# Kernel optimization log

Measured on AMD Instinct MI355X. Metric: run time of the kernel, lower is better.

## Reference

```python
import jax, jax.numpy as jnp
import numpy as np

N_DST = 25000
E = 400000
DN = 128   # dim_node
DE = 128   # dim_edge
DT = 128   # dim_time
DO = 128   # dim_out
H = 2      # num_head


def setup_inputs() -> dict:
    key = jax.random.key(0)
    ks = jax.random.split(key, 10)
    sc = 0.05
    node_h = jax.random.normal(ks[0], (N_DST + E, DN), jnp.float32)
    edge_f = jax.random.normal(ks[1], (E, DE), jnp.float32)
    dt = jax.random.uniform(ks[2], (E,), jnp.float32) * 100.0
    dst_idx = jax.random.randint(ks[3], (E,), 0, N_DST)
    # TimeEncode: Linear(1, dim_time) with w initialized to 1/10**linspace(0,9)
    time_w = jnp.asarray(1.0 / 10 ** np.linspace(0, 9, DT, dtype=np.float32))
    time_b = jnp.zeros((DT,), jnp.float32)
    Wq = jax.random.normal(ks[4], (DO, DN + DT), jnp.float32) * sc
    bq = jnp.zeros((DO,), jnp.float32)
    Wk = jax.random.normal(ks[5], (DO, DN + DE + DT), jnp.float32) * sc
    bk = jnp.zeros((DO,), jnp.float32)
    Wv = jax.random.normal(ks[6], (DO, DN + DE + DT), jnp.float32) * sc
    bv = jnp.zeros((DO,), jnp.float32)
    Wout = jax.random.normal(ks[7], (DO, DN + DO), jnp.float32) * sc
    bout = jnp.zeros((DO,), jnp.float32)
    gamma = jnp.ones((DO,), jnp.float32)
    beta = jnp.zeros((DO,), jnp.float32)
    return dict(node_h=node_h, edge_f=edge_f, dt=dt, dst_idx=dst_idx,
                time_w=time_w, time_b=time_b, Wq=Wq, bq=bq, Wk=Wk, bk=bk,
                Wv=Wv, bv=bv, Wout=Wout, bout=bout, gamma=gamma, beta=beta)


def reference(node_h, edge_f, dt, dst_idx, time_w, time_b,
              Wq, bq, Wk, bk, Wv, bv, Wout, bout, gamma, beta):
    num_dst = node_h.shape[0] - edge_f.shape[0]
    num_edges = edge_f.shape[0]
    tgt = node_h[:num_dst]            # [N, DN] target node embeddings
    src = node_h[num_dst:]            # [E, DN] per-edge source embeddings

    # TimeEncode: cos(w * dt + b)
    time_feats = jnp.cos(dt[:, None] * time_w[None, :] + time_b)          # [E, DT]
    zero_time = jnp.broadcast_to(jnp.cos(time_b), (num_dst, time_b.shape[0]))

    Qn = jnp.concatenate([tgt, zero_time], axis=1) @ Wq.T + bq            # [N, DO]
    kv_in = jnp.concatenate([src, edge_f, time_feats], axis=1)            # [E, DN+DE+DT]
    K = kv_in @ Wk.T + bk                                                 # [E, DO]
    V = kv_in @ Wv.T + bv                                                 # [E, DO]
    Q = Qn[dst_idx]                                                       # gather per edge

    d_head = Q.shape[1] // H
    Qh = Q.reshape(num_edges, H, d_head)
    Kh = K.reshape(num_edges, H, d_head)
    Vh = V.reshape(num_edges, H, d_head)

    score = jnp.sum(Qh * Kh, axis=2)                                      # [E, H]
    score = jnp.where(score >= 0, score, 0.2 * score)                     # LeakyReLU(0.2)

    # edge_softmax: segmented softmax over incoming edges of each dst node
    m = jax.ops.segment_max(score, dst_idx, num_segments=num_dst)
    m = jnp.where(jnp.isfinite(m), m, 0.0)                                # empty segments
    e = jnp.exp(score - m[dst_idx])
    s = jax.ops.segment_sum(e, dst_idx, num_segments=num_dst)
    att = e / s[dst_idx]                                                  # [E, H]

    Vw = (Vh * att[:, :, None]).reshape(num_edges, -1)                    # [E, DO]
    h = jax.ops.segment_sum(Vw, dst_idx, num_segments=num_dst)            # scatter-sum

    rst = jnp.concatenate([h, tgt], axis=1) @ Wout.T + bout               # [N, DO]
    rst = jax.nn.relu(rst)
    mu = jnp.mean(rst, axis=-1, keepdims=True)
    var = jnp.var(rst, axis=-1, keepdims=True)
    return (rst - mu) / jnp.sqrt(var + 1e-5) * gamma + beta
```

## Files before the change

### kernel.cpp

```cpp
#include <hip/hip_runtime.h>

#define N_DST 25000
#define E_NUM 400000

typedef __bf16 bf16x8 __attribute__((ext_vector_type(8)));
typedef __bf16 bf16x4 __attribute__((ext_vector_type(4)));
typedef __bf16 bf16x2 __attribute__((ext_vector_type(2)));
typedef float  f32x4  __attribute__((ext_vector_type(4)));

__device__ __forceinline__ float fast_cos(float x) {
  float r = x * 0.15915494309189535f;
  r = r - floorf(r);
  return __builtin_amdgcn_cosf(r);
}

__device__ __forceinline__ void gload_lds16(const void* g, void* l) {
  __builtin_amdgcn_global_load_lds(
      (const __attribute__((address_space(1))) unsigned int*)g,
      (__attribute__((address_space(3))) unsigned int*)l, 16, 0, 0);
}

#define PIPE_WAIT(S)                         \
  do {                                       \
    __builtin_amdgcn_sched_barrier(0);       \
    asm volatile(S ::: "memory");            \
    __builtin_amdgcn_sched_barrier(0);       \
    __builtin_amdgcn_s_barrier();            \
    __builtin_amdgcn_sched_barrier(0);       \
  } while (0)

__device__ __forceinline__ void pack_frag(const float* __restrict__ W0,
    const float* __restrict__ W1, int stride, int NC, int idx, __bf16* __restrict__ out) {
  int lane = idx & 63, fid = idx >> 6;
  int nfw = NC >> 6;
  int perks = nfw << 2;
  int ks = fid / perks, rem = fid - ks * perks;
  int w = rem / nfw, nf = rem - w * nfw;
  int n = w * (NC >> 2) + nf * 16 + (lane & 15);
  int g = (ks << 2) + (lane >> 4);
  const float* src = (W1 && n >= 128) ? (W1 + (size_t)(n - 128) * stride)
                                      : (W0 + (size_t)n * stride);
  const float4* s4 = reinterpret_cast<const float4*>(src + g * 8);
  float4 lo = s4[0], hi = s4[1];
  bf16x8 b;
  b[0]=(__bf16)lo.x; b[1]=(__bf16)lo.y; b[2]=(__bf16)lo.z; b[3]=(__bf16)lo.w;
  b[4]=(__bf16)hi.x; b[5]=(__bf16)hi.y; b[6]=(__bf16)hi.z; b[7]=(__bf16)hi.w;
  reinterpret_cast<bf16x8*>(out)[idx] = b;
}

__global__ __launch_bounds__(256) void prep_kernel(
    const float* __restrict__ Wq, const float* __restrict__ bq, const float* __restrict__ tb,
    const float* __restrict__ Wk, const float* __restrict__ Wv, const float* __restrict__ Wout,
    const int* __restrict__ dsti,
    float* __restrict__ cq, __bf16* __restrict__ Bq_kv, __bf16* __restrict__ Bq_q,
    __bf16* __restrict__ Bq_out, int* __restrict__ counts) {
  int b = blockIdx.x, tid = threadIdx.x;
  if (b == 0) {
    if (tid < 128) {
      float s = bq[tid];
      for (int j = 0; j < 128; ++j) s += cosf(tb[j]) * Wq[tid * 256 + 128 + j];
      cq[tid] = s;
    }
    return;
  }
  b -= 1;
  if (b < 48) { pack_frag(Wk, Wv, 384, 256, b * 256 + tid, Bq_kv); return; }
  b -= 48;
  if (b < 8)  { pack_frag(Wq, nullptr, 256, 128, b * 256 + tid, Bq_q); return; }
  b -= 8;
  if (b < 16) { pack_frag(Wout, nullptr, 256, 128, b * 256 + tid, Bq_out); return; }
  b -= 16;
  int e = b * 256 + tid;
  if (e < E_NUM) atomicAdd(&counts[dsti[e]], 1);
}

__global__ __launch_bounds__(1024) void scan_kernel(const int* __restrict__ counts,
    int* __restrict__ offs, int* __restrict__ cursor) {
  __shared__ int wpart[16];
  int tid = threadIdx.x, lane = tid & 63, wid = tid >> 6;
  int carry = 0;
  for (int base = 0; base < N_DST; base += 1024) {
    int idx = base + tid;
    int x = (idx < N_DST) ? counts[idx] : 0;
    int incl = x;
#pragma unroll
    for (int o = 1; o < 64; o <<= 1) {
      int y = __shfl_up(incl, o);
      if (lane >= o) incl += y;
    }
    if (lane == 63) wpart[wid] = incl;
    __syncthreads();
    if (wid == 0) {
      int v = (lane < 16) ? wpart[lane] : 0;
      int s = v;
#pragma unroll
      for (int o = 1; o < 16; o <<= 1) {
        int y = __shfl_up(s, o);
        if (lane >= o) s += y;
      }
      if (lane < 16) wpart[lane] = s;
    }
    __syncthreads();
    int woff = (wid > 0) ? wpart[wid - 1] : 0;
    int tot = wpart[15];
    if (idx < N_DST) {
      int v = carry + woff + incl - x;
      offs[idx] = v;
      cursor[idx] = v;
    }
    carry += tot;
    __syncthreads();
  }
  if (tid == 0) offs[N_DST] = carry;
}

__global__ __launch_bounds__(256) void fill_kernel(const int* __restrict__ dsti,
    int* __restrict__ cursor, int* __restrict__ pos) {
  int e = blockIdx.x * 256 + threadIdx.x;
  if (e < E_NUM) {
    int d = dsti[e];
    int p = atomicAdd(&cursor[d], 1);
    pos[e] = p;
  }
}

__global__ __launch_bounds__(256, 3) void kv_kernel(
    const float* __restrict__ node_h, const float* __restrict__ edge_f,
    const float* __restrict__ dtp, const float* __restrict__ tw, const float* __restrict__ tb,
    const __bf16* __restrict__ Bq,
    const float* __restrict__ bk, const float* __restrict__ bv,
    const int* __restrict__ dsti, const int* __restrict__ pos,
    const float* __restrict__ Qn,
    __bf16* __restrict__ Vout, float* __restrict__ score)
{
  __shared__ __align__(16) float Abuf[3][4096];
  __shared__ int Dlds[64];
  __shared__ int Plds[64];
  __shared__ float dts[64];
  __shared__ float twl[128];
  __shared__ float tbl[128];

  const int tid = threadIdx.x;
  const int e0 = blockIdx.x * 64;
  const int lane = tid & 63;
  const int w = tid >> 6;
  const int lrow = lane & 15;
  const int lk = lane >> 4;
  const int aswz = (lrow & 7) << 4;

  if (tid < 64) {
    Dlds[tid] = dsti[e0 + tid];
    Plds[tid] = pos[e0 + tid];
    dts[tid] = dtp[e0 + tid];
  } else if (tid < 192) {
    int j = tid - 64;
    twl[j] = tw[j];
    tbl[j] = tb[j];
  }
  __syncthreads();

  auto stage_mem = [&](int t, int bufi) {
    const char* base;
    if (t < 2) base = (const char*)(node_h + ((size_t)(N_DST + e0)) * 128 + t * 64);
    else       base = (const char*)(edge_f + (size_t)e0 * 128 + (t - 2) * 64);
#pragma unroll
    for (int i = 0; i < 4; ++i) {
      int g = w * 4 + i;
      int r = g * 4 + (lane >> 4);
      int srcoff = r * 512 + ((((lane & 15) << 4)) ^ ((r & 7) << 4));
      gload_lds16(base + srcoff, &Abuf[bufi][g * 256]);
    }
  };
  auto stage_cos = [&](int t, float* buf) {
    int r = tid >> 2;
    int j0 = (tid & 3) << 4;
    float d = dts[r];
    int swz = (r & 7) << 4;
    char* rowb = (char*)(buf + r * 64);
#pragma unroll
    for (int q = 0; q < 4; ++q) {
      f32x4 vv;
#pragma unroll
      for (int jj = 0; jj < 4; ++jj) {
        int J = (t - 4) * 64 + j0 + q * 4 + jj;
        vv[jj] = fast_cos(d * twl[J] + tbl[J]);
      }
      *reinterpret_cast<f32x4*>(rowb + (((j0 << 2) + (q << 4)) ^ swz)) = vv;
    }
  };

  f32x4 acc[4][4];
#pragma unroll
  for (int mf = 0; mf < 4; ++mf)
#pragma unroll
    for (int nf = 0; nf < 4; ++nf)
      acc[mf][nf] = (f32x4){0.f, 0.f, 0.f, 0.f};

  const bf16x8* __restrict__ Bw = reinterpret_cast<const bf16x8*>(Bq) + (size_t)(w * 4) * 64 + lane;

  auto ktile = [&](const float* buf, int t) {
#pragma unroll
    for (int ks = 0; ks < 2; ++ks) {
      int K32 = t * 2 + ks;
      bf16x8 b[4];
#pragma unroll
      for (int nf = 0; nf < 4; ++nf)
        b[nf] = Bw[((size_t)K32 * 16 + nf) * 64];
      bf16x8 a[4];
#pragma unroll
      for (int mf = 0; mf < 4; ++mf) {
        const char* rowb = (const char*)(buf + (mf * 16 + lrow) * 64);
        int cb = ks * 128 + lk * 32;
        f32x4 f0 = *reinterpret_cast<const f32x4*>(rowb + (cb ^ aswz));
        f32x4 f1 = *reinterpret_cast<const f32x4*>(rowb + ((cb + 16) ^ aswz));
        bf16x8 av;
#pragma unroll
        for (int j = 0; j < 4; ++j) {
          av[j] = (__bf16)f0[j];
          av[4 + j] = (__bf16)f1[j];
        }
        a[mf] = av;
      }
#pragma unroll
      for (int nf = 0; nf < 4; ++nf)
#pragma unroll
        for (int mf = 0; mf < 4; ++mf)
          acc[mf][nf] = __builtin_amdgcn_mfma_f32_16x16x32_bf16(a[mf], b[nf], acc[mf][nf], 0, 0, 0);
    }
  };

  stage_mem(0, 0);
  stage_mem(1, 1);
  PIPE_WAIT("s_waitcnt vmcnt(4)");
  stage_mem(2, 2); ktile(Abuf[0], 0);
  PIPE_WAIT("s_waitcnt vmcnt(4)");
  stage_mem(3, 0); ktile(Abuf[1], 1);
  PIPE_WAIT("s_waitcnt vmcnt(4)");
  stage_cos(4, Abuf[1]); ktile(Abuf[2], 2);
  PIPE_WAIT("s_waitcnt vmcnt(0) lgkmcnt(0)");
  stage_cos(5, Abuf[2]); ktile(Abuf[0], 3);
  PIPE_WAIT("s_waitcnt lgkmcnt(0)");
  ktile(Abuf[1], 4);
  ktile(Abuf[2], 5);

  char* Vlds = (char*)Abuf[0];
  if (w >= 2) {
#pragma unroll
    for (int nf = 0; nf < 4; ++nf) {
      int vcol = (w - 2) * 64 + nf * 16 + lrow;
      float bb = bv[vcol];
#pragma unroll
      for (int mf = 0; mf < 4; ++mf) {
#pragma unroll
        for (int r = 0; r < 4; ++r) {
          int row = mf * 16 + lk * 4 + r;
          *reinterpret_cast<__bf16*>(Vlds + row * 256 + ((vcol * 2) ^ ((row & 7) << 4))) =
              (__bf16)(acc[mf][nf][r] + bb);
        }
      }
    }
  } else {
    float bkv[4];
#pragma unroll
    for (int nf = 0; nf < 4; ++nf) bkv[nf] = bk[w * 64 + nf * 16 + lrow];
#pragma unroll
    for (int mf = 0; mf < 4; ++mf) {
#pragma unroll
      for (int r = 0; r < 4; ++r) {
        int row = mf * 16 + lk * 4 + r;
        const float* qrow = Qn + ((size_t)Dlds[row] << 7) + w * 64;
        float s = 0.f;
#pragma unroll
        for (int nf = 0; nf < 4; ++nf)
          s += (acc[mf][nf][r] + bkv[nf]) * qrow[nf * 16 + lrow];
        s += __shfl_xor(s, 1);
        s += __shfl_xor(s, 2);
        s += __shfl_xor(s, 4);
        s += __shfl_xor(s, 8);
        if (lrow == 0) {
          s = (s >= 0.f) ? s : 0.2f * s;
          score[((size_t)Plds[row] << 1) + w] = s;
        }
      }
    }
  }
  __syncthreads();
#pragma unroll
  for (int i = 0; i < 4; ++i) {
    int c = tid + i * 256;
    int r = c >> 4, cb = (c & 15) << 4;
    bf16x8 vv = *reinterpret_cast<const bf16x8*>(Vlds + r * 256 + (cb ^ ((r & 7) << 4)));
    *reinterpret_cast<bf16x8*>(Vout + (((size_t)Plds[r]) << 7) + (c & 15) * 8) = vv;
  }
}

template<int MODE>
__global__ __launch_bounds__(256, 4) void gemm_kernel(
    const float* __restrict__ A0, const float* __restrict__ A1,
    const float* __restrict__ dtp, const float* __restrict__ tw,
    const __bf16* __restrict__ Bq, const float* __restrict__ bias0,
    float* __restrict__ outF)
{
  constexpr int NC = 128;
  constexpr int NFRAGW = 2;
  __shared__ __align__(16) char Abuf[2][64 * 256];

  const int tid = threadIdx.x;
  const int e0 = blockIdx.x * 64;
  const int nv = min(64, N_DST - e0);
  const int srow = tid >> 5;
  const int sc4 = (tid & 31) << 2;

  const int lane = tid & 63;
  const int w = tid >> 6;
  const int nbase = w * (NC / 4);
  const int lrow = lane & 15;
  const int lk = lane >> 4;
  const int aswz = (lrow & 7) << 4;
  const bf16x8* __restrict__ Bw =
      reinterpret_cast<const bf16x8*>(Bq) + (size_t)(w * NFRAGW) * 64 + lane;

  f32x4 acc[4][NFRAGW];
#pragma unroll
  for (int mf = 0; mf < 4; ++mf)
#pragma unroll
    for (int nf = 0; nf < NFRAGW; ++nf)
      acc[mf][nf] = (f32x4){0.f, 0.f, 0.f, 0.f};

  auto issueA = [&](int t, float4 (&v)[8]) {
    const float* base = (t == 0) ? A0 : A1;
#pragma unroll
    for (int i = 0; i < 8; ++i) {
      int r = srow + i * 8;
      v[i] = (r < nv) ? *reinterpret_cast<const float4*>(base + (size_t)(e0 + r) * 128 + sc4)
                      : make_float4(0.f, 0.f, 0.f, 0.f);
    }
  };
  auto writeA = [&](char* buf, float4 (&v)[8]) {
#pragma unroll
    for (int i = 0; i < 8; ++i) {
      int r = srow + i * 8;
      bf16x4 b;
      b[0]=(__bf16)v[i].x; b[1]=(__bf16)v[i].y; b[2]=(__bf16)v[i].z; b[3]=(__bf16)v[i].w;
      *reinterpret_cast<bf16x4*>(buf + r * 256 + ((sc4 * 2) ^ ((r & 7) << 4))) = b;
    }
  };
  auto ktile = [&](const char* buf, int t) {
#pragma unroll
    for (int ks = 0; ks < 4; ++ks) {
      bf16x8 b[NFRAGW];
#pragma unroll
      for (int nf = 0; nf < NFRAGW; ++nf)
        b[nf] = Bw[((size_t)(t * 4 + ks) * 4 * NFRAGW + nf) * 64];
      bf16x8 a[4];
#pragma unroll
      for (int mf = 0; mf < 4; ++mf)
        a[mf] = *reinterpret_cast<const bf16x8*>(
            buf + (mf * 16 + lrow) * 256 + (((ks * 32 + lk * 8) * 2) ^ aswz));
#pragma unroll
      for (int nf = 0; nf < NFRAGW; ++nf)
#pragma unroll
        for (int mf = 0; mf < 4; ++mf)
          acc[mf][nf] = __builtin_amdgcn_mfma_f32_16x16x32_bf16(a[mf], b[nf], acc[mf][nf], 0, 0, 0);
    }
  };

  float4 v[8];
  issueA(0, v);
  writeA(Abuf[0], v);
  __syncthreads();
  if constexpr (MODE == 2) {
    issueA(1, v);
    ktile(Abuf[0], 0);
    writeA(Abuf[1], v);
    __syncthreads();
    ktile(Abuf[1], 1);
  } else {
    ktile(Abuf[0], 0);
  }

  if constexpr (MODE == 0) {
#pragma unroll
    for (int nf = 0; nf < NFRAGW; ++nf) {
      int col = nbase + nf * 16 + lrow;
      float bb = bias0[col];
#pragma unroll
      for (int mf = 0; mf < 4; ++mf) {
#pragma unroll
        for (int r = 0; r < 4; ++r) {
          int row = mf * 16 + lk * 4 + r;
          if (row < nv)
            outF[(size_t)(e0 + row) * 128 + col] = acc[mf][nf][r] + bb;
        }
      }
    }
  } else {
    const float* gammaP = dtp;
    const float* betaP = tw;
    float vals[NFRAGW][4][4];
#pragma unroll
    for (int nf = 0; nf < NFRAGW; ++nf) {
      float bb = bias0[nbase + nf * 16 + lrow];
#pragma unroll
      for (int mf = 0; mf < 4; ++mf)
#pragma unroll
        for (int r = 0; r < 4; ++r)
          vals[nf][mf][r] = fmaxf(acc[mf][nf][r] + bb, 0.f);
    }
    __syncthreads();
    float* sums = reinterpret_cast<float*>(Abuf[0]);
    float* sqs  = reinterpret_cast<float*>(Abuf[0]) + 256;
    float* stats = reinterpret_cast<float*>(Abuf[0]) + 512;
#pragma unroll
    for (int mf = 0; mf < 4; ++mf) {
#pragma unroll
      for (int r = 0; r < 4; ++r) {
        float s1 = vals[0][mf][r] + vals[1][mf][r];
        float s2 = vals[0][mf][r] * vals[0][mf][r] + vals[1][mf][r] * vals[1][mf][r];
#pragma unroll
        for (int o = 1; o < 16; o <<= 1) {
          s1 += __shfl_xor(s1, o);
          s2 += __shfl_xor(s2, o);
        }
        if (lrow == 0) {
          int row = mf * 16 + lk * 4 + r;
          sums[w * 64 + row] = s1;
          sqs[w * 64 + row] = s2;
        }
      }
    }
    __syncthreads();
    if (tid < 64) {
      float s = sums[tid] + sums[64 + tid] + sums[128 + tid] + sums[192 + tid];
      float q = sqs[tid] + sqs[64 + tid] + sqs[128 + tid] + sqs[192 + tid];
      float mean = s * (1.f / 128.f);
      float var = q * (1.f / 128.f) - mean * mean;
      stats[tid * 2] = mean;
      stats[tid * 2 + 1] = rsqrtf(var + 1e-5f);
    }
    __syncthreads();
#pragma unroll
    for (int nf = 0; nf < NFRAGW; ++nf) {
      int col = nbase + nf * 16 + lrow;
      float g = gammaP[col], bC = betaP[col];
#pragma unroll
      for (int mf = 0; mf < 4; ++mf) {
#pragma unroll
        for (int r = 0; r < 4; ++r) {
          int row = mf * 16 + lk * 4 + r;
          if (row < nv) {
            float mean = stats[row * 2], rs = stats[row * 2 + 1];
            outF[(size_t)(e0 + row) * 128 + col] = (vals[nf][mf][r] - mean) * rs * g + bC;
          }
        }
      }
    }
  }
}

__global__ __launch_bounds__(256) void agg_kernel(const int* __restrict__ offs,
    const float* __restrict__ score, const __bf16* __restrict__ V, float* __restrict__ h) {
  int d = blockIdx.x * 4 + (threadIdx.x >> 6);
  if (d >= N_DST) return;
  int lane = threadIdx.x & 63;
  int beg = offs[d], end = offs[d + 1];
  int n = end - beg;
  float m0 = -3.0e38f, m1 = -3.0e38f;
  for (int i = lane; i < n; i += 64) {
    float2 sc = *reinterpret_cast<const float2*>(score + 2 * (size_t)(beg + i));
    m0 = fmaxf(m0, sc.x); m1 = fmaxf(m1, sc.y);
  }
#pragma unroll
  for (int o = 32; o; o >>= 1) {
    m0 = fmaxf(m0, __shfl_xor(m0, o));
    m1 = fmaxf(m1, __shfl_xor(m1, o));
  }
  float s0 = 0.f, s1 = 0.f;
  for (int i = lane; i < n; i += 64) {
    float2 sc = *reinterpret_cast<const float2*>(score + 2 * (size_t)(beg + i));
    s0 += __expf(sc.x - m0); s1 += __expf(sc.y - m1);
  }
#pragma unroll
  for (int o = 32; o; o >>= 1) {
    s0 += __shfl_xor(s0, o);
    s1 += __shfl_xor(s1, o);
  }
  float inv0 = (n > 0) ? 1.f / s0 : 0.f;
  float inv1 = (n > 0) ? 1.f / s1 : 0.f;
  int q = lane >> 4, j = lane & 15;
  int hsel = j >> 3;
  float acc[8];
#pragma unroll
  for (int k2 = 0; k2 < 8; ++k2) acc[k2] = 0.f;
  for (int i0 = 0; i0 < n; i0 += 4) {
    int i = i0 + q;
    if (i < n) {
      size_t p = beg + i;
      float2 sc = *reinterpret_cast<const float2*>(score + 2 * p);
      float wgt = hsel ? __expf(sc.y - m1) * inv1 : __expf(sc.x - m0) * inv0;
      bf16x8 v = *reinterpret_cast<const bf16x8*>(V + (p << 7) + j * 8);
#pragma unroll
      for (int k2 = 0; k2 < 8; ++k2) acc[k2] += wgt * (float)v[k2];
    }
  }
#pragma unroll
  for (int k2 = 0; k2 < 8; ++k2) {
    acc[k2] += __shfl_xor(acc[k2], 16);
    acc[k2] += __shfl_xor(acc[k2], 32);
  }
  if (q == 0) {
    float4 lo = make_float4(acc[0], acc[1], acc[2], acc[3]);
    float4 hi = make_float4(acc[4], acc[5], acc[6], acc[7]);
    float* dst = h + ((size_t)d << 7) + j * 8;
    *reinterpret_cast<float4*>(dst) = lo;
    *reinterpret_cast<float4*>(dst + 4) = hi;
  }
}

extern "C" void kernel_launch(void* const* d_in, const int* in_sizes, int n_in,
                              void* d_out, int out_size, void* d_ws, size_t ws_size,
                              hipStream_t stream) {
  (void)in_sizes; (void)n_in; (void)out_size; (void)ws_size;
  const float* node_h = (const float*)d_in[0];
  const float* edge_f = (const float*)d_in[1];
  const float* dtp    = (const float*)d_in[2];
  const int*   dsti   = (const int*)d_in[3];
  const float* tw     = (const float*)d_in[4];
  const float* tb     = (const float*)d_in[5];
  const float* Wq     = (const float*)d_in[6];
  const float* bq     = (const float*)d_in[7];
  const float* Wk     = (const float*)d_in[8];
  const float* bk     = (const float*)d_in[9];
  const float* Wv     = (const float*)d_in[10];
  const float* bv     = (const float*)d_in[11];
  const float* Wout   = (const float*)d_in[12];
  const float* bout   = (const float*)d_in[13];
  const float* gamma  = (const float*)d_in[14];
  const float* beta   = (const float*)d_in[15];
  float* outp = (float*)d_out;

  size_t off = 0;
  auto take = [&](size_t nbytes) -> void* {
    void* r = (char*)d_ws + off;
    off += (nbytes + 255) & ~(size_t)255;
    return r;
  };
  __bf16* Bq_kv  = (__bf16*)take((size_t)12288 * 16);
  __bf16* Bq_q   = (__bf16*)take((size_t)2048 * 16);
  __bf16* Bq_out = (__bf16*)take((size_t)4096 * 16);
  float*  cq     = (float*)take(128 * 4);
  float*  Qn     = (float*)take((size_t)N_DST * 128 * 4);
  __bf16* Vbuf   = (__bf16*)take((size_t)E_NUM * 128 * 2);
  float*  score  = (float*)take((size_t)E_NUM * 2 * 4);
  int*    counts = (int*)take((size_t)N_DST * 4);
  int*    offs   = (int*)take((size_t)(N_DST + 1) * 4);
  int*    cursor = (int*)take((size_t)N_DST * 4);
  int*    pos    = (int*)take((size_t)E_NUM * 4);
  float*  hbuf   = (float*)take((size_t)N_DST * 128 * 4);

  hipMemsetAsync(counts, 0, (size_t)N_DST * 4, stream);

  const int count_blocks = (E_NUM + 255) / 256;
  prep_kernel<<<1 + 48 + 8 + 16 + count_blocks, 256, 0, stream>>>(
      Wq, bq, tb, Wk, Wv, Wout, dsti, cq, Bq_kv, Bq_q, Bq_out, counts);

  gemm_kernel<0><<<(N_DST + 63) / 64, 256, 0, stream>>>(node_h, nullptr, nullptr, nullptr,
      Bq_q, cq, Qn);

  scan_kernel<<<1, 1024, 0, stream>>>(counts, offs, cursor);
  fill_kernel<<<count_blocks, 256, 0, stream>>>(dsti, cursor, pos);

  kv_kernel<<<E_NUM / 64, 256, 0, stream>>>(node_h, edge_f, dtp, tw, tb,
      Bq_kv, bk, bv, dsti, pos, Qn, Vbuf, score);

  agg_kernel<<<(N_DST + 3) / 4, 256, 0, stream>>>(offs, score, Vbuf, hbuf);

  gemm_kernel<2><<<(N_DST + 63) / 64, 256, 0, stream>>>(hbuf, node_h, gamma, beta,
      Bq_out, bout, outp);
}
```

Baseline: 360.2 us.

## Load KV GEMM A-operands directly from global; split scan into three-phase parallel kernels

The KV kernel drops its triple-buffered LDS pipeline (global_load_lds with waitcnt/barrier staging) and instead reads the source and edge feature fragments straight from global memory into registers. The time-encoding cosines are precomputed once into a small bf16 LDS tile. This cuts LDS from 48KB to 16KB, which is meant to raise occupancy, but the direct loads are strided per row and may coalesce worse, with less explicit latency hiding. Separately, the single-block serial scan becomes a three-kernel reduce/offset/scan spread over 25 blocks, at the cost of two extra launches.

After: 468.6 us. +30.1%, slower.

```diff
diff --git a/kernel.cpp b/kernel.cpp
--- a/kernel.cpp
+++ b/kernel.cpp
@@ -13,21 +13,6 @@
   r = r - floorf(r);
   return __builtin_amdgcn_cosf(r);
 }
-
-__device__ __forceinline__ void gload_lds16(const void* g, void* l) {
-  __builtin_amdgcn_global_load_lds(
-      (const __attribute__((address_space(1))) unsigned int*)g,
-      (__attribute__((address_space(3))) unsigned int*)l, 16, 0, 0);
-}
-
-#define PIPE_WAIT(S)                         \
-  do {                                       \
-    __builtin_amdgcn_sched_barrier(0);       \
-    asm volatile(S ::: "memory");            \
-    __builtin_amdgcn_sched_barrier(0);       \
-    __builtin_amdgcn_s_barrier();            \
-    __builtin_amdgcn_sched_barrier(0);       \
-  } while (0)
 
 __device__ __forceinline__ void pack_frag(const float* __restrict__ W0,
     const float* __restrict__ W1, int stride, int NC, int idx, __bf16* __restrict__ out) {
@@ -74,44 +59,64 @@
   if (e < E_NUM) atomicAdd(&counts[dsti[e]], 1);
 }
 
-__global__ __launch_bounds__(1024) void scan_kernel(const int* __restrict__ counts,
-    int* __restrict__ offs, int* __restrict__ cursor) {
+__global__ __launch_bounds__(1024) void scanA_kernel(const int* __restrict__ counts,
+    int* __restrict__ bsum) {
+  __shared__ int wsum[16];
+  int tid = threadIdx.x;
+  int idx = blockIdx.x * 1024 + tid;
+  int s = (idx < N_DST) ? counts[idx] : 0;
+#pragma unroll
+  for (int o = 32; o; o >>= 1) s += __shfl_xor(s, o);
+  if ((tid & 63) == 0) wsum[tid >> 6] = s;
+  __syncthreads();
+  if (tid == 0) {
+    int t = 0;
+#pragma unroll
+    for (int i = 0; i < 16; ++i) t += wsum[i];
+    bsum[blockIdx.x] = t;
+  }
+}
+
+__global__ void scanB_kernel(const int* __restrict__ bsum, int* __restrict__ boff) {
+  if (threadIdx.x == 0) {
+    int c = 0;
+    for (int i = 0; i < 25; ++i) { boff[i] = c; c += bsum[i]; }
+    boff[25] = c;
+  }
+}
+
+__global__ __launch_bounds__(1024) void scanC_kernel(const int* __restrict__ counts,
+    const int* __restrict__ boff, int* __restrict__ offs, int* __restrict__ cursor) {
   __shared__ int wpart[16];
   int tid = threadIdx.x, lane = tid & 63, wid = tid >> 6;
-  int carry = 0;
-  for (int base = 0; base < N_DST; base += 1024) {
-    int idx = base + tid;
-    int x = (idx < N_DST) ? counts[idx] : 0;
-    int incl = x;
-#pragma unroll
-    for (int o = 1; o < 64; o <<= 1) {
-      int y = __shfl_up(incl, o);
-      if (lane >= o) incl += y;
-    }
-    if (lane == 63) wpart[wid] = incl;
-    __syncthreads();
-    if (wid == 0) {
-      int v = (lane < 16) ? wpart[lane] : 0;
-      int s = v;
-#pragma unroll
-      for (int o = 1; o < 16; o <<= 1) {
-        int y = __shfl_up(s, o);
-        if (lane >= o) s += y;
-      }
-      if (lane < 16) wpart[lane] = s;
-    }
-    __syncthreads();
-    int woff = (wid > 0) ? wpart[wid - 1] : 0;
-    int tot = wpart[15];
-    if (idx < N_DST) {
-      int v = carry + woff + incl - x;
-      offs[idx] = v;
-      cursor[idx] = v;
-    }
-    carry += tot;
-    __syncthreads();
-  }
-  if (tid == 0) offs[N_DST] = carry;
+  int idx = blockIdx.x * 1024 + tid;
+  int x = (idx < N_DST) ? counts[idx] : 0;
+  int incl = x;
+#pragma unroll
+  for (int o = 1; o < 64; o <<= 1) {
+    int y = __shfl_up(incl, o);
+    if (lane >= o) incl += y;
+  }
+  if (lane == 63) wpart[wid] = incl;
+  __syncthreads();
+  if (wid == 0) {
+    int v = (lane < 16) ? wpart[lane] : 0;
+    int s = v;
+#pragma unroll
+    for (int o = 1; o < 16; o <<= 1) {
+      int y = __shfl_up(s, o);
+      if (lane >= o) s += y;
+    }
+    if (lane < 16) wpart[lane] = s;
+  }
+  __syncthreads();
+  int woff = (wid > 0) ? wpart[wid - 1] : 0;
+  int v = boff[blockIdx.x] + woff + incl - x;
+  if (idx < N_DST) {
+    offs[idx] = v;
+    cursor[idx] = v;
+  }
+  if (idx == N_DST - 1) offs[N_DST] = v + x;
 }
 
 __global__ __launch_bounds__(256) void fill_kernel(const int* __restrict__ dsti,
@@ -133,7 +138,7 @@
     const float* __restrict__ Qn,
     __bf16* __restrict__ Vout, float* __restrict__ score)
 {
-  __shared__ __align__(16) float Abuf[3][4096];
+  __shared__ __align__(16) char Cbuf[64 * 256];
   __shared__ int Dlds[64];
   __shared__ int Plds[64];
   __shared__ float dts[64];
@@ -159,35 +164,24 @@
   }
   __syncthreads();
 
-  auto stage_mem = [&](int t, int bufi) {
-    const char* base;
-    if (t < 2) base = (const char*)(node_h + ((size_t)(N_DST + e0)) * 128 + t * 64);
-    else       base = (const char*)(edge_f + (size_t)e0 * 128 + (t - 2) * 64);
-#pragma unroll
-    for (int i = 0; i < 4; ++i) {
-      int g = w * 4 + i;
-      int r = g * 4 + (lane >> 4);
-      int srcoff = r * 512 + ((((lane & 15) << 4)) ^ ((r & 7) << 4));
-      gload_lds16(base + srcoff, &Abuf[bufi][g * 256]);
-    }
-  };
-  auto stage_cos = [&](int t, float* buf) {
+  {
     int r = tid >> 2;
-    int j0 = (tid & 3) << 4;
     float d = dts[r];
+    int jb = (tid & 3) << 5;
+    char* rowb = Cbuf + r * 256;
     int swz = (r & 7) << 4;
-    char* rowb = (char*)(buf + r * 64);
-#pragma unroll
-    for (int q = 0; q < 4; ++q) {
-      f32x4 vv;
-#pragma unroll
-      for (int jj = 0; jj < 4; ++jj) {
-        int J = (t - 4) * 64 + j0 + q * 4 + jj;
-        vv[jj] = fast_cos(d * twl[J] + tbl[J]);
-      }
-      *reinterpret_cast<f32x4*>(rowb + (((j0 << 2) + (q << 4)) ^ swz)) = vv;
-    }
-  };
+#pragma unroll
+    for (int c = 0; c < 4; ++c) {
+      bf16x8 p;
+#pragma unroll
+      for (int jj = 0; jj < 8; ++jj) {
+        int J = jb + c * 8 + jj;
+        p[jj] = (__bf16)fast_cos(d * twl[J] + tbl[J]);
+      }
+      *reinterpret_cast<bf16x8*>(rowb + (((jb + c * 8) * 2) ^ swz)) = p;
+    }
+  }
+  __syncthreads();
 
   f32x4 acc[4][4];
 #pragma unroll
@@ -197,53 +191,45 @@
       acc[mf][nf] = (f32x4){0.f, 0.f, 0.f, 0.f};
 
   const bf16x8* __restrict__ Bw = reinterpret_cast<const bf16x8*>(Bq) + (size_t)(w * 4) * 64 + lane;
-
-  auto ktile = [&](const float* buf, int t) {
-#pragma unroll
-    for (int ks = 0; ks < 2; ++ks) {
-      int K32 = t * 2 + ks;
-      bf16x8 b[4];
-#pragma unroll
-      for (int nf = 0; nf < 4; ++nf)
-        b[nf] = Bw[((size_t)K32 * 16 + nf) * 64];
-      bf16x8 a[4];
+  const float* __restrict__ srcb = node_h + ((size_t)(N_DST + e0)) * 128 + lk * 8;
+  const float* __restrict__ edgb = edge_f + (size_t)e0 * 128 + lk * 8;
+
+#pragma unroll
+  for (int K32 = 0; K32 < 12; ++K32) {
+    bf16x8 a[4];
+    if (K32 < 8) {
+      const float* base = (K32 < 4) ? (srcb + K32 * 32) : (edgb + (K32 - 4) * 32);
 #pragma unroll
       for (int mf = 0; mf < 4; ++mf) {
-        const char* rowb = (const char*)(buf + (mf * 16 + lrow) * 64);
-        int cb = ks * 128 + lk * 32;
-        f32x4 f0 = *reinterpret_cast<const f32x4*>(rowb + (cb ^ aswz));
-        f32x4 f1 = *reinterpret_cast<const f32x4*>(rowb + ((cb + 16) ^ aswz));
+        const float* p = base + (size_t)(mf * 16 + lrow) * 128;
+        f32x4 f0 = *reinterpret_cast<const f32x4*>(p);
+        f32x4 f1 = *reinterpret_cast<const f32x4*>(p + 4);
         bf16x8 av;
 #pragma unroll
-        for (int j = 0; j < 4; ++j) {
-          av[j] = (__bf16)f0[j];
-          av[4 + j] = (__bf16)f1[j];
-        }
+        for (int j = 0; j < 4; ++j) { av[j] = (__bf16)f0[j]; av[4 + j] = (__bf16)f1[j]; }
         a[mf] = av;
       }
-#pragma unroll
-      for (int nf = 0; nf < 4; ++nf)
-#pragma unroll
-        for (int mf = 0; mf < 4; ++mf)
-          acc[mf][nf] = __builtin_amdgcn_mfma_f32_16x16x32_bf16(a[mf], b[nf], acc[mf][nf], 0, 0, 0);
-    }
-  };
-
-  stage_mem(0, 0);
-  stage_mem(1, 1);
-  PIPE_WAIT("s_waitcnt vmcnt(4)");
-  stage_mem(2, 2); ktile(Abuf[0], 0);
-  PIPE_WAIT("s_waitcnt vmcnt(4)");
-  stage_mem(3, 0); ktile(Abuf[1], 1);
-  PIPE_WAIT("s_waitcnt vmcnt(4)");
-  stage_cos(4, Abuf[1]); ktile(Abuf[2], 2);
-  PIPE_WAIT("s_waitcnt vmcnt(0) lgkmcnt(0)");
-  stage_cos(5, Abuf[2]); ktile(Abuf[0], 3);
-  PIPE_WAIT("s_waitcnt lgkmcnt(0)");
-  ktile(Abuf[1], 4);
-  ktile(Abuf[2], 5);
-
-  char* Vlds = (char*)Abuf[0];
+    } else {
+#pragma unroll
+      for (int mf = 0; mf < 4; ++mf) {
+        int row = mf * 16 + lrow;
+        a[mf] = *reinterpret_cast<const bf16x8*>(
+            Cbuf + row * 256 + ((((K32 - 8) * 32 + lk * 8) * 2) ^ aswz));
+      }
+    }
+    bf16x8 b[4];
+#pragma unroll
+    for (int nf = 0; nf < 4; ++nf)
+      b[nf] = Bw[((size_t)K32 * 16 + nf) * 64];
+#pragma unroll
+    for (int nf = 0; nf < 4; ++nf)
+#pragma unroll
+      for (int mf = 0; mf < 4; ++mf)
+        acc[mf][nf] = __builtin_amdgcn_mfma_f32_16x16x32_bf16(a[mf], b[nf], acc[mf][nf], 0, 0, 0);
+  }
+
+  __syncthreads();
+  char* Vlds = Cbuf;
   if (w >= 2) {
 #pragma unroll
     for (int nf = 0; nf < 4; ++nf) {
@@ -556,6 +542,8 @@
   int*    offs   = (int*)take((size_t)(N_DST + 1) * 4);
   int*    cursor = (int*)take((size_t)N_DST * 4);
   int*    pos    = (int*)take((size_t)E_NUM * 4);
+  int*    bsum   = (int*)take(32 * 4);
+  int*    boff   = (int*)take(32 * 4);
   float*  hbuf   = (float*)take((size_t)N_DST * 128 * 4);
 
   hipMemsetAsync(counts, 0, (size_t)N_DST * 4, stream);
@@ -567,7 +555,9 @@
   gemm_kernel<0><<<(N_DST + 63) / 64, 256, 0, stream>>>(node_h, nullptr, nullptr, nullptr,
       Bq_q, cq, Qn);
 
-  scan_kernel<<<1, 1024, 0, stream>>>(counts, offs, cursor);
+  scanA_kernel<<<25, 1024, 0, stream>>>(counts, bsum);
+  scanB_kernel<<<1, 64, 0, stream>>>(bsum, boff);
+  scanC_kernel<<<25, 1024, 0, stream>>>(counts, boff, offs, cursor);
   fill_kernel<<<count_blocks, 256, 0, stream>>>(dsti, cursor, pos);
 
   kv_kernel<<<E_NUM / 64, 256, 0, stream>>>(node_h, edge_f, dtp, tw, tb,
```
